# Performance work log

Hardware: AMD Instinct MI355X
Metric: run time of the kernel (lower is better)

The kernel has to match this reference:

```python
import jax, jax.numpy as jnp
import numpy as np

B, C, N = 2, 512, 2048
HEADS, DIM_HEAD, SCALE = 16, 64, 8.0
H_DIM = HEADS * DIM_HEAD
EPS = 1e-12  # F.normalize default eps


def setup_inputs() -> dict:
    key = jax.random.key(0)
    ks = jax.random.split(key, 5)
    x = jax.random.normal(ks[0], (B, C, N), dtype=jnp.float32)
    Wqkv = jax.random.normal(ks[1], (3 * H_DIM, C), dtype=jnp.float32) * (1.0 / np.sqrt(C))
    q_scale = jnp.ones((DIM_HEAD,), dtype=jnp.float32)
    k_scale = jnp.ones((DIM_HEAD,), dtype=jnp.float32)
    Wout = jax.random.normal(ks[2], (C, H_DIM), dtype=jnp.float32) * (1.0 / np.sqrt(H_DIM))
    bout = jax.random.normal(ks[3], (C,), dtype=jnp.float32) * 0.01
    return {"x": x, "Wqkv": Wqkv, "q_scale": q_scale, "k_scale": k_scale,
            "Wout": Wout, "bout": bout}


def _l2norm(t):
    # F.normalize(t, dim=-1): t / max(||t||, eps)
    n = jnp.sqrt(jnp.sum(t * t, axis=-1, keepdims=True))
    return t / jnp.maximum(n, EPS)


def reference(x, Wqkv, q_scale, k_scale, Wout, bout):
    # 1x1 conv == pointwise matmul over channel dim
    qkv = jnp.einsum('oc,bcn->bon', Wqkv, x)              # [B, 3*H_DIM, N]
    q, k, v = jnp.split(qkv, 3, axis=1)
    # unflatten channels -> [B, H, D, N]
    def to_heads(t):
        return t.reshape(B, HEADS, DIM_HEAD, N)
    q, k, v = map(to_heads, (q, k, v))
    # cosine attention: l2-normalize q,k over head dim, apply learned per-dim scales
    q = _l2norm(q.transpose(0, 1, 3, 2)) * q_scale        # [B, H, N, D]
    k = _l2norm(k.transpose(0, 1, 3, 2)) * k_scale        # [B, H, N, D]
    sim = jnp.einsum('bhid,bhjd->bhij', q, k) * SCALE     # [B, H, N, N]
    attn = jax.nn.softmax(sim, axis=-1)
    out = jnp.einsum('bhij,bhdj->bhid', attn, v)          # [B, H, N, D]
    out = out.transpose(0, 1, 3, 2).reshape(B, H_DIM, N)  # b h n d -> b (h d) n
    return jnp.einsum('oc,bcn->bon', Wout, out) + bout[None, :, None]
```

## Files before the change

kernel.cpp:

```cpp
#include <hip/hip_runtime.h>
#include <hip/hip_bf16.h>

#define BATCH 2
#define CCH   512
#define NSEQ  2048
#define HEADS 16
#define DHEAD 64
#define HDIM  1024
#define ODIM  3072
#define QK_PRESCALE 11.541560327111707f

typedef short short4v __attribute__((ext_vector_type(4)));
typedef short short8 __attribute__((ext_vector_type(8)));
typedef float float4v __attribute__((ext_vector_type(4)));

__device__ __forceinline__ unsigned short f2bf(float f) {
    unsigned int u = __float_as_uint(f);
    return (unsigned short)((u + 0x7FFFu + ((u >> 16) & 1u)) >> 16);
}
__device__ __forceinline__ unsigned short f2bf_fast(float f) {
    return (unsigned short)((__float_as_uint(f) + 0x8000u) >> 16);
}
__device__ __forceinline__ float fexp2(float x) {
#if __has_builtin(__builtin_amdgcn_exp2f)
    return __builtin_amdgcn_exp2f(x);
#else
    return exp2f(x);
#endif
}

typedef __attribute__((address_space(1))) const void* as1_cvp;
typedef __attribute__((address_space(3))) void* as3_vp;
__device__ __forceinline__ void cp16(const void* g, void* l) {
    __builtin_amdgcn_global_load_lds((as1_cvp)g, (as3_vp)l, 16, 0, 0);
}

__global__ __launch_bounds__(256) void k_convert_w(
    const float* __restrict__ Wqkv, const float* __restrict__ Wout,
    const float* __restrict__ qs, const float* __restrict__ ks,
    unsigned short* __restrict__ Wqkvb, unsigned short* __restrict__ Woutb,
    float* __restrict__ M) {
    if (blockIdx.x == 0 && threadIdx.x < 64) {
        int lane = threadIdx.x;
        float p = fabsf(qs[lane] * ks[lane]);
#pragma unroll
        for (int off = 1; off < 64; off <<= 1) p = fmaxf(p, __shfl_xor(p, off));
        if (lane == 0) *M = QK_PRESCALE * p;
    }
    int i4 = (blockIdx.x * 256 + threadIdx.x) * 4;
    const float* src; unsigned short* dst; int idx;
    if (i4 < ODIM * CCH) { src = Wqkv; dst = Wqkvb; idx = i4; }
    else { src = Wout; dst = Woutb; idx = i4 - ODIM * CCH; }
    float4 v = *(const float4*)(src + idx);
    ushort4 o;
    o.x = f2bf(v.x); o.y = f2bf(v.y); o.z = f2bf(v.z); o.w = f2bf(v.w);
    *(ushort4*)(dst + idx) = o;
}

__global__ __launch_bounds__(256) void k_transpose_x(
    const float* __restrict__ x, unsigned short* __restrict__ xt) {
    __shared__ unsigned short t[64][65];
    const int b = blockIdx.z, c0 = blockIdx.y * 64, n0 = blockIdx.x * 64;
    const int tr = threadIdx.x >> 6, tc = threadIdx.x & 63;
    const float* xs = x + (size_t)b * CCH * NSEQ;
    unsigned short* xd = xt + (size_t)b * NSEQ * CCH;
#pragma unroll
    for (int r = 0; r < 16; ++r) {
        int c = r * 4 + tr;
        t[c][tc] = f2bf(xs[(size_t)(c0 + c) * NSEQ + n0 + tc]);
    }
    __syncthreads();
#pragma unroll
    for (int r = 0; r < 16; ++r) {
        int n = r * 4 + tr;
        xd[(size_t)(n0 + n) * CCH + c0 + tc] = t[tc][n];
    }
}

__global__ __launch_bounds__(256) void k_gemm_qkv(
    const unsigned short* __restrict__ W, const unsigned short* __restrict__ xt,
    const float* __restrict__ qs, const float* __restrict__ ks,
    unsigned short* __restrict__ qh, unsigned short* __restrict__ kh,
    unsigned short* __restrict__ vb) {
    constexpr int K = CCH, N = NSEQ;
    __shared__ __align__(16) short smem[2 * 128 * 64];
    short* lsA = smem;
    short* lsB = smem + 128 * 64;
    const int tid = threadIdx.x, wave = tid >> 6, lane = tid & 63;
    const int l15 = lane & 15, quad = lane >> 4;
    const int n0 = blockIdx.x * 128, m0 = blockIdx.y * 128, z = blockIdx.z;
    const short* Ab = (const short*)W + (size_t)m0 * K;
    const short* Bb = (const short*)xt + ((size_t)z * N + n0) * K;
    const int wm = wave >> 1, wn = wave & 1;
    const int cswz = (((tid & 7) ^ ((tid >> 3) & 7))) * 8;
    const int sw7 = (l15 & 7);

    float4v acc[4][4];
#pragma unroll
    for (int i = 0; i < 4; ++i)
#pragma unroll
        for (int j = 0; j < 4; ++j) acc[i][j] = (float4v){0.f, 0.f, 0.f, 0.f};

    for (int k0 = 0; k0 < K; k0 += 64) {
#pragma unroll
        for (int it = 0; it < 4; ++it) {
            int row = it * 32 + (tid >> 3);
            cp16(Ab + (size_t)row * K + k0 + cswz, &lsA[it * 2048 + wave * 512]);
            cp16(Bb + (size_t)row * K + k0 + cswz, &lsB[it * 2048 + wave * 512]);
        }
        __syncthreads();
        short8 af[4][2], bfr[4][2];
#pragma unroll
        for (int t = 0; t < 4; ++t)
#pragma unroll
            for (int kk = 0; kk < 2; ++kk) {
                af[t][kk]  = *(const short8*)&lsA[(wm * 64 + t * 16 + l15) * 64 + ((kk * 4 + quad) ^ sw7) * 8];
                bfr[t][kk] = *(const short8*)&lsB[(wn * 64 + t * 16 + l15) * 64 + ((kk * 4 + quad) ^ sw7) * 8];
            }
#pragma unroll
        for (int mt = 0; mt < 4; ++mt)
#pragma unroll
            for (int nt = 0; nt < 4; ++nt) {
                acc[mt][nt] = __builtin_amdgcn_mfma_f32_16x16x32_bf16(af[mt][0], bfr[nt][0], acc[mt][nt], 0, 0, 0);
                acc[mt][nt] = __builtin_amdgcn_mfma_f32_16x16x32_bf16(af[mt][1], bfr[nt][1], acc[mt][nt], 0, 0, 0);
            }
        __syncthreads();
    }

    const int co   = (m0 + wm * 64) >> 6;
    const int part = co >> 4;
    const int h    = co & 15;
    const int bh   = z * HEADS + h;
    short* myT = smem + wave * 4096;

    if (part < 2) {
        float inv[4];
#pragma unroll
        for (int nt = 0; nt < 4; ++nt) {
            float ss = 0.f;
#pragma unroll
            for (int mt = 0; mt < 4; ++mt)
#pragma unroll
                for (int r = 0; r < 4; ++r) ss += acc[mt][nt][r] * acc[mt][nt][r];
            ss += __shfl_xor(ss, 16);
            ss += __shfl_xor(ss, 32);
            inv[nt] = 1.0f / fmaxf(sqrtf(ss), 1e-12f);
        }
        const float* sc = part ? ks : qs;
        const float csc = part ? 1.0f : QK_PRESCALE;
#pragma unroll
        for (int mt = 0; mt < 4; ++mt) {
            const int db = mt * 16 + quad * 4;
            float4 s4 = *(const float4*)(sc + db);
            s4.x *= csc; s4.y *= csc; s4.z *= csc; s4.w *= csc;
#pragma unroll
            for (int nt = 0; nt < 4; ++nt) {
                int nl = nt * 16 + l15;
                short4v o;
                o.x = (short)f2bf(acc[mt][nt][0] * inv[nt] * s4.x);
                o.y = (short)f2bf(acc[mt][nt][1] * inv[nt] * s4.y);
                o.z = (short)f2bf(acc[mt][nt][2] * inv[nt] * s4.z);
                o.w = (short)f2bf(acc[mt][nt][3] * inv[nt] * s4.w);
                *(short4v*)&myT[nl * 64 + (((db >> 3) ^ (nl & 7)) << 3) + (db & 7)] = o;
            }
        }
        unsigned short* dst = (part ? kh : qh) + (size_t)bh * NSEQ * DHEAD
                              + (size_t)(n0 + wn * 64) * DHEAD;
#pragma unroll
        for (int pass = 0; pass < 8; ++pass) {
            int nl = pass * 8 + (lane >> 3), c = lane & 7;
            short8 vv = *(const short8*)&myT[nl * 64 + ((c ^ (nl & 7)) << 3)];
            *(short8*)&dst[(size_t)nl * DHEAD + c * 8] = vv;
        }
    } else {
#pragma unroll
        for (int mt = 0; mt < 4; ++mt)
#pragma unroll
            for (int nt = 0; nt < 4; ++nt) {
                int nl = nt * 16 + l15;
                int swc = nl >> 3, swo = nl & 7;
#pragma unroll
                for (int r = 0; r < 4; ++r) {
                    int d = mt * 16 + quad * 4 + r;
                    myT[d * 64 + ((swc ^ (d & 7)) << 3) + swo] = (short)f2bf(acc[mt][nt][r]);
                }
            }
        unsigned short* dst = vb + (size_t)bh * DHEAD * NSEQ + n0 + wn * 64;
#pragma unroll
        for (int pass = 0; pass < 8; ++pass) {
            int d = pass * 8 + (lane >> 3), c = lane & 7;
            short8 vv = *(const short8*)&myT[d * 64 + ((c ^ (d & 7)) << 3)];
            *(short8*)&dst[(size_t)d * NSEQ + c * 8] = vv;
        }
    }
}

__global__ __launch_bounds__(256, 4) void k_attn(
    const unsigned short* __restrict__ qh, const unsigned short* __restrict__ kh,
    const unsigned short* __restrict__ vb,
    unsigned short* __restrict__ aot, const float* __restrict__ Mptr) {
    __shared__ __align__(16) short Kt[2][64 * 64];
    __shared__ __align__(16) short Vt[2][64 * 64];
    __shared__ __align__(16) short Pt[64 * 64];
    const int tid = threadIdx.x, wave = tid >> 6, lane = tid & 63;
    const int l15 = lane & 15, quad = lane >> 4, q8 = quad * 8;
    const int flat = blockIdx.x;
    const int xcd = flat & 7, idx = flat >> 3;
    const int bh = xcd * 4 + (idx >> 5);
    const int i0 = (idx & 31) * 64;
    const int b = bh >> 4, h = bh & 15;
    const float Ms = *Mptr;
    const float4v mInit = (float4v){-Ms, -Ms, -Ms, -Ms};
    const int cswz = (((tid & 7) ^ ((tid >> 3) & 7))) * 8;
    const int sw7 = (l15 & 7);
    const int srow = tid >> 3;

    short8 qf[2];
    {
        const short* qb = (const short*)qh + ((size_t)bh * NSEQ + i0 + wave * 16) * DHEAD;
        qf[0] = *(const short8*)&qb[l15 * DHEAD + q8];
        qf[1] = *(const short8*)&qb[l15 * DHEAD + 32 + q8];
    }

    float4v of[4];
#pragma unroll
    for (int dt = 0; dt < 4; ++dt) of[dt] = (float4v){0.f, 0.f, 0.f, 0.f};
    float l_acc[4] = {0.f, 0.f, 0.f, 0.f};

    const short* kbase = (const short*)kh + (size_t)bh * NSEQ * DHEAD;
    const short* vbase = (const short*)vb + (size_t)bh * DHEAD * NSEQ;
    short* myP = Pt + wave * 1024;

#pragma unroll
    for (int it = 0; it < 2; ++it) {
        int row = it * 32 + srow;
        cp16(kbase + (size_t)row * DHEAD + cswz, &Kt[0][it * 2048 + wave * 512]);
        cp16(vbase + (size_t)row * NSEQ + cswz, &Vt[0][it * 2048 + wave * 512]);
    }
    __syncthreads();

    int buf = 0;
    for (int j0 = 0; j0 < NSEQ; j0 += 64) {
        if (j0 + 64 < NSEQ) {
            int nb = buf ^ 1;
#pragma unroll
            for (int it = 0; it < 2; ++it) {
                int row = it * 32 + srow;
                cp16(kbase + (size_t)(j0 + 64 + row) * DHEAD + cswz, &Kt[nb][it * 2048 + wave * 512]);
                cp16(vbase + (size_t)row * NSEQ + j0 + 64 + cswz, &Vt[nb][it * 2048 + wave * 512]);
            }
        }

        float4v s[4];
#pragma unroll
        for (int nt = 0; nt < 4; ++nt) {
            short8 kf0 = *(const short8*)&Kt[buf][(nt * 16 + l15) * 64 + ((0 + quad) ^ sw7) * 8];
            short8 kf1 = *(const short8*)&Kt[buf][(nt * 16 + l15) * 64 + ((4 + quad) ^ sw7) * 8];
            float4v zz = mInit;
            zz = __builtin_amdgcn_mfma_f32_16x16x32_bf16(qf[0], kf0, zz, 0, 0, 0);
            zz = __builtin_amdgcn_mfma_f32_16x16x32_bf16(qf[1], kf1, zz, 0, 0, 0);
            s[nt] = zz;
        }

#pragma unroll
        for (int r = 0; r < 4; ++r) {
            int prow = quad * 4 + r;
            int psw = prow & 7;
            float p0 = fexp2(s[0][r]);
            float p1 = fexp2(s[1][r]);
            float p2 = fexp2(s[2][r]);
            float p3 = fexp2(s[3][r]);
            l_acc[r] += (p0 + p1) + (p2 + p3);
            myP[prow * 64 + (((0 + (l15 >> 3)) ^ psw) * 8) + (l15 & 7)] = (short)f2bf_fast(p0);
            myP[prow * 64 + (((2 + (l15 >> 3)) ^ psw) * 8) + (l15 & 7)] = (short)f2bf_fast(p1);
            myP[prow * 64 + (((4 + (l15 >> 3)) ^ psw) * 8) + (l15 & 7)] = (short)f2bf_fast(p2);
            myP[prow * 64 + (((6 + (l15 >> 3)) ^ psw) * 8) + (l15 & 7)] = (short)f2bf_fast(p3);
        }

        short8 af0 = *(const short8*)&myP[l15 * 64 + ((0 + quad) ^ sw7) * 8];
        short8 af1 = *(const short8*)&myP[l15 * 64 + ((4 + quad) ^ sw7) * 8];
#pragma unroll
        for (int dt = 0; dt < 4; ++dt) {
            short8 vf0 = *(const short8*)&Vt[buf][(dt * 16 + l15) * 64 + ((0 + quad) ^ sw7) * 8];
            short8 vf1 = *(const short8*)&Vt[buf][(dt * 16 + l15) * 64 + ((4 + quad) ^ sw7) * 8];
            of[dt] = __builtin_amdgcn_mfma_f32_16x16x32_bf16(af0, vf0, of[dt], 0, 0, 0);
            of[dt] = __builtin_amdgcn_mfma_f32_16x16x32_bf16(af1, vf1, of[dt], 0, 0, 0);
        }

        __syncthreads();
        buf ^= 1;
    }

#pragma unroll
    for (int r = 0; r < 4; ++r) {
        float l = l_acc[r];
        l += __shfl_xor(l, 1); l += __shfl_xor(l, 2);
        l += __shfl_xor(l, 4); l += __shfl_xor(l, 8);
        l_acc[r] = 1.0f / fmaxf(l, 1e-30f);
    }

    unsigned short* ob = aot + ((size_t)b * NSEQ + i0 + wave * 16) * HDIM + h * DHEAD;
#pragma unroll
    for (int dt = 0; dt < 4; ++dt)
#pragma unroll
        for (int r = 0; r < 4; ++r)
            ob[(size_t)(quad * 4 + r) * HDIM + dt * 16 + l15] = f2bf(of[dt][r] * l_acc[r]);
}

__global__ __launch_bounds__(256) void k_gemm_out(
    const unsigned short* __restrict__ W, const unsigned short* __restrict__ aot,
    const float* __restrict__ bias, float* __restrict__ out) {
    constexpr int K = HDIM, N = NSEQ, M = CCH;
    __shared__ __align__(16) short lsA[64 * 64];
    __shared__ __align__(16) short lsB[64 * 64];
    const int tid = threadIdx.x, wave = tid >> 6, lane = tid & 63;
    const int l15 = lane & 15, quad = lane >> 4;
    const int n0 = blockIdx.x * 64, m0 = blockIdx.y * 64, z = blockIdx.z;
    const short* Ab = (const short*)W + (size_t)m0 * K;
    const short* Bb = (const short*)aot + ((size_t)z * N + n0) * K;
    const int wm = wave >> 1, wn = wave & 1;
    const int cswz = (((tid & 7) ^ ((tid >> 3) & 7))) * 8;
    const int sw7 = (l15 & 7);

    float4v acc[2][2];
#pragma unroll
    for (int i = 0; i < 2; ++i)
#pragma unroll
        for (int j = 0; j < 2; ++j) acc[i][j] = (float4v){0.f, 0.f, 0.f, 0.f};

    for (int k0 = 0; k0 < K; k0 += 64) {
        {
            int row = tid >> 3;
            cp16(Ab + (size_t)row * K + k0 + cswz, &lsA[wave * 512]);
            cp16(Ab + (size_t)(row + 32) * K + k0 + cswz, &lsA[2048 + wave * 512]);
            cp16(Bb + (size_t)row * K + k0 + cswz, &lsB[wave * 512]);
            cp16(Bb + (size_t)(row + 32) * K + k0 + cswz, &lsB[2048 + wave * 512]);
        }
        __syncthreads();
        short8 af[2][2], bfr[2][2];
#pragma unroll
        for (int t = 0; t < 2; ++t)
#pragma unroll
            for (int kk = 0; kk < 2; ++kk) {
                af[t][kk]  = *(const short8*)&lsA[(wm * 32 + t * 16 + l15) * 64 + ((kk * 4 + quad) ^ sw7) * 8];
                bfr[t][kk] = *(const short8*)&lsB[(wn * 32 + t * 16 + l15) * 64 + ((kk * 4 + quad) ^ sw7) * 8];
            }
#pragma unroll
        for (int mt = 0; mt < 2; ++mt)
#pragma unroll
            for (int nt = 0; nt < 2; ++nt) {
                acc[mt][nt] = __builtin_amdgcn_mfma_f32_16x16x32_bf16(af[mt][0], bfr[nt][0], acc[mt][nt], 0, 0, 0);
                acc[mt][nt] = __builtin_amdgcn_mfma_f32_16x16x32_bf16(af[mt][1], bfr[nt][1], acc[mt][nt], 0, 0, 0);
            }
        __syncthreads();
    }
    float* Co = out + (size_t)z * M * N;
#pragma unroll
    for (int mt = 0; mt < 2; ++mt)
#pragma unroll
        for (int nt = 0; nt < 2; ++nt) {
            int mrow = m0 + wm * 32 + mt * 16 + quad * 4;
#pragma unroll
            for (int r = 0; r < 4; ++r) {
                int mr = mrow + r;
                int nc = n0 + wn * 32 + nt * 16 + l15;
                Co[(size_t)mr * N + nc] = acc[mt][nt][r] + bias[mr];
            }
        }
}

extern "C" void kernel_launch(void* const* d_in, const int* in_sizes, int n_in,
                              void* d_out, int out_size, void* d_ws, size_t ws_size,
                              hipStream_t stream) {
    const float* x = nullptr; const float* Wqkv = nullptr;
    const float* qs = nullptr; const float* ks = nullptr;
    const float* Wout = nullptr; const float* bout = nullptr;
    for (int i = 0; i < n_in; ++i) {
        switch (in_sizes[i]) {
            case BATCH * CCH * NSEQ: x    = (const float*)d_in[i]; break;
            case ODIM * CCH:         Wqkv = (const float*)d_in[i]; break;
            case CCH * HDIM:         Wout = (const float*)d_in[i]; break;
            case CCH:                bout = (const float*)d_in[i]; break;
            case DHEAD: if (!qs) qs = (const float*)d_in[i]; else ks = (const float*)d_in[i]; break;
            default: break;
        }
    }
    float* y = (float*)d_out;

    char* ws = (char*)d_ws;
    float*          Mbuf  = (float*)(ws + 0);
    unsigned short* Wqkvb = (unsigned short*)(ws + 4096);
    unsigned short* Woutb = (unsigned short*)(ws + 3149824);
    unsigned short* xt    = (unsigned short*)(ws + 4198400);
    unsigned short* qh    = (unsigned short*)(ws + 8392704);
    unsigned short* kh    = (unsigned short*)(ws + 16781312);
    unsigned short* vb    = (unsigned short*)(ws + 25169920);
    unsigned short* aot   = (unsigned short*)(ws + 33558528);

    k_convert_w<<<(ODIM * CCH + CCH * HDIM) / 4 / 256, 256, 0, stream>>>(
        Wqkv, Wout, qs, ks, Wqkvb, Woutb, Mbuf);
    k_transpose_x<<<dim3(NSEQ / 64, CCH / 64, BATCH), 256, 0, stream>>>(x, xt);
    k_gemm_qkv<<<dim3(NSEQ / 128, ODIM / 128, BATCH), 256, 0, stream>>>(Wqkvb, xt, qs, ks, qh, kh, vb);
    k_attn<<<dim3(1024), 256, 0, stream>>>(qh, kh, vb, aot, Mbuf);
    k_gemm_out<<<dim3(NSEQ / 64, CCH / 64, BATCH), 256, 0, stream>>>(Woutb, aot, bout, y);
}
```

Before: 171.0 us.

## Double attention query tile per block and fuse weight-convert with x-transpose

The attention kernel now gives each block 128 query rows, two 16-row m-tiles per wave, so every K/V tile staged in LDS is reused across twice as many queries. This halves the block count and the K/V global and LDS traffic per query. In exchange it uses more registers and LDS per block, and the occupancy hint drops from 4 to 2. Separately, the weight-conversion and x-transpose kernels are merged into one launch to save a kernel launch.

```diff
diff --git a/kernel.cpp b/kernel.cpp
--- a/kernel.cpp
+++ b/kernel.cpp
@@ -35,32 +35,36 @@
     __builtin_amdgcn_global_load_lds((as1_cvp)g, (as3_vp)l, 16, 0, 0);
 }
 
-__global__ __launch_bounds__(256) void k_convert_w(
+__global__ __launch_bounds__(256) void k_prep(
     const float* __restrict__ Wqkv, const float* __restrict__ Wout,
+    const float* __restrict__ x,
     const float* __restrict__ qs, const float* __restrict__ ks,
     unsigned short* __restrict__ Wqkvb, unsigned short* __restrict__ Woutb,
-    float* __restrict__ M) {
-    if (blockIdx.x == 0 && threadIdx.x < 64) {
-        int lane = threadIdx.x;
-        float p = fabsf(qs[lane] * ks[lane]);
-#pragma unroll
-        for (int off = 1; off < 64; off <<= 1) p = fmaxf(p, __shfl_xor(p, off));
-        if (lane == 0) *M = QK_PRESCALE * p;
-    }
-    int i4 = (blockIdx.x * 256 + threadIdx.x) * 4;
-    const float* src; unsigned short* dst; int idx;
-    if (i4 < ODIM * CCH) { src = Wqkv; dst = Wqkvb; idx = i4; }
-    else { src = Wout; dst = Woutb; idx = i4 - ODIM * CCH; }
-    float4 v = *(const float4*)(src + idx);
-    ushort4 o;
-    o.x = f2bf(v.x); o.y = f2bf(v.y); o.z = f2bf(v.z); o.w = f2bf(v.w);
-    *(ushort4*)(dst + idx) = o;
-}
-
-__global__ __launch_bounds__(256) void k_transpose_x(
-    const float* __restrict__ x, unsigned short* __restrict__ xt) {
+    unsigned short* __restrict__ xt, float* __restrict__ M) {
+    const int bx = blockIdx.x;
+    if (bx < 2048) {
+        if (bx == 0 && threadIdx.x < 64) {
+            int lane = threadIdx.x;
+            float p = fabsf(qs[lane] * ks[lane]);
+#pragma unroll
+            for (int off = 1; off < 64; off <<= 1) p = fmaxf(p, __shfl_xor(p, off));
+            if (lane == 0) *M = QK_PRESCALE * p;
+        }
+        int i4 = (bx * 256 + threadIdx.x) * 4;
+        const float* src; unsigned short* dst; int idx;
+        if (i4 < ODIM * CCH) { src = Wqkv; dst = Wqkvb; idx = i4; }
+        else { src = Wout; dst = Woutb; idx = i4 - ODIM * CCH; }
+        float4 v = *(const float4*)(src + idx);
+        ushort4 o;
+        o.x = f2bf(v.x); o.y = f2bf(v.y); o.z = f2bf(v.z); o.w = f2bf(v.w);
+        *(ushort4*)(dst + idx) = o;
+        return;
+    }
     __shared__ unsigned short t[64][65];
-    const int b = blockIdx.z, c0 = blockIdx.y * 64, n0 = blockIdx.x * 64;
+    const int fx = bx - 2048;
+    const int n0 = (fx & 31) * 64;
+    const int c0 = ((fx >> 5) & 7) * 64;
+    const int b  = fx >> 8;
     const int tr = threadIdx.x >> 6, tc = threadIdx.x & 63;
     const float* xs = x + (size_t)b * CCH * NSEQ;
     unsigned short* xd = xt + (size_t)b * NSEQ * CCH;
@@ -195,19 +199,19 @@
     }
 }
 
-__global__ __launch_bounds__(256, 4) void k_attn(
+__global__ __launch_bounds__(256, 2) void k_attn(
     const unsigned short* __restrict__ qh, const unsigned short* __restrict__ kh,
     const unsigned short* __restrict__ vb,
     unsigned short* __restrict__ aot, const float* __restrict__ Mptr) {
     __shared__ __align__(16) short Kt[2][64 * 64];
     __shared__ __align__(16) short Vt[2][64 * 64];
-    __shared__ __align__(16) short Pt[64 * 64];
+    __shared__ __align__(16) short Pt[128 * 64];
     const int tid = threadIdx.x, wave = tid >> 6, lane = tid & 63;
     const int l15 = lane & 15, quad = lane >> 4, q8 = quad * 8;
     const int flat = blockIdx.x;
     const int xcd = flat & 7, idx = flat >> 3;
-    const int bh = xcd * 4 + (idx >> 5);
-    const int i0 = (idx & 31) * 64;
+    const int bh = xcd * 4 + (idx >> 4);
+    const int i0 = (idx & 15) * 128;
     const int b = bh >> 4, h = bh & 15;
     const float Ms = *Mptr;
     const float4v mInit = (float4v){-Ms, -Ms, -Ms, -Ms};
@@ -215,21 +219,29 @@
     const int sw7 = (l15 & 7);
     const int srow = tid >> 3;
 
-    short8 qf[2];
+    short8 qf[2][2];
     {
-        const short* qb = (const short*)qh + ((size_t)bh * NSEQ + i0 + wave * 16) * DHEAD;
-        qf[0] = *(const short8*)&qb[l15 * DHEAD + q8];
-        qf[1] = *(const short8*)&qb[l15 * DHEAD + 32 + q8];
-    }
-
-    float4v of[4];
-#pragma unroll
-    for (int dt = 0; dt < 4; ++dt) of[dt] = (float4v){0.f, 0.f, 0.f, 0.f};
-    float l_acc[4] = {0.f, 0.f, 0.f, 0.f};
+        const short* qb = (const short*)qh + ((size_t)bh * NSEQ + i0 + wave * 32) * DHEAD;
+#pragma unroll
+        for (int mt = 0; mt < 2; ++mt) {
+            qf[mt][0] = *(const short8*)&qb[(mt * 16 + l15) * DHEAD + q8];
+            qf[mt][1] = *(const short8*)&qb[(mt * 16 + l15) * DHEAD + 32 + q8];
+        }
+    }
+
+    float4v of[2][4];
+#pragma unroll
+    for (int mt = 0; mt < 2; ++mt)
+#pragma unroll
+        for (int dt = 0; dt < 4; ++dt) of[mt][dt] = (float4v){0.f, 0.f, 0.f, 0.f};
+    float l_acc[2][4];
+#pragma unroll
+    for (int mt = 0; mt < 2; ++mt)
+#pragma unroll
+        for (int r = 0; r < 4; ++r) l_acc[mt][r] = 0.f;
 
     const short* kbase = (const short*)kh + (size_t)bh * NSEQ * DHEAD;
     const short* vbase = (const short*)vb + (size_t)bh * DHEAD * NSEQ;
-    short* myP = Pt + wave * 1024;
 
 #pragma unroll
     for (int it = 0; it < 2; ++it) {
@@ -251,40 +263,53 @@
             }
         }
 
-        float4v s[4];
+        float4v s[2][4];
 #pragma unroll
         for (int nt = 0; nt < 4; ++nt) {
             short8 kf0 = *(const short8*)&Kt[buf][(nt * 16 + l15) * 64 + ((0 + quad) ^ sw7) * 8];
             short8 kf1 = *(const short8*)&Kt[buf][(nt * 16 + l15) * 64 + ((4 + quad) ^ sw7) * 8];
-            float4v zz = mInit;
-            zz = __builtin_amdgcn_mfma_f32_16x16x32_bf16(qf[0], kf0, zz, 0, 0, 0);
-            zz = __builtin_amdgcn_mfma_f32_16x16x32_bf16(qf[1], kf1, zz, 0, 0, 0);
-            s[nt] = zz;
-        }
-
-#pragma unroll
-        for (int r = 0; r < 4; ++r) {
-            int prow = quad * 4 + r;
-            int psw = prow & 7;
-            float p0 = fexp2(s[0][r]);
-            float p1 = fexp2(s[1][r]);
-            float p2 = fexp2(s[2][r]);
-            float p3 = fexp2(s[3][r]);
-            l_acc[r] += (p0 + p1) + (p2 + p3);
-            myP[prow * 64 + (((0 + (l15 >> 3)) ^ psw) * 8) + (l15 & 7)] = (short)f2bf_fast(p0);
-            myP[prow * 64 + (((2 + (l15 >> 3)) ^ psw) * 8) + (l15 & 7)] = (short)f2bf_fast(p1);
-            myP[prow * 64 + (((4 + (l15 >> 3)) ^ psw) * 8) + (l15 & 7)] = (short)f2bf_fast(p2);
-            myP[prow * 64 + (((6 + (l15 >> 3)) ^ psw) * 8) + (l15 & 7)] = (short)f2bf_fast(p3);
-        }
-
-        short8 af0 = *(const short8*)&myP[l15 * 64 + ((0 + quad) ^ sw7) * 8];
-        short8 af1 = *(const short8*)&myP[l15 * 64 + ((4 + quad) ^ sw7) * 8];
+#pragma unroll
+            for (int mt = 0; mt < 2; ++mt) {
+                float4v zz = mInit;
+                zz = __builtin_amdgcn_mfma_f32_16x16x32_bf16(qf[mt][0], kf0, zz, 0, 0, 0);
+                zz = __builtin_amdgcn_mfma_f32_16x16x32_bf16(qf[mt][1], kf1, zz, 0, 0, 0);
+                s[mt][nt] = zz;
+            }
+        }
+
+#pragma unroll
+        for (int mt = 0; mt < 2; ++mt)
+#pragma unroll
+            for (int r = 0; r < 4; ++r) {
+                int prow = wave * 32 + mt * 16 + quad * 4 + r;
+                int psw = prow & 7;
+                float p0 = fexp2(s[mt][0][r]);
+                float p1 = fexp2(s[mt][1][r]);
+                float p2 = fexp2(s[mt][2][r]);
+                float p3 = fexp2(s[mt][3][r]);
+                l_acc[mt][r] += (p0 + p1) + (p2 + p3);
+                Pt[prow * 64 + (((0 + (l15 >> 3)) ^ psw) * 8) + (l15 & 7)] = (short)f2bf_fast(p0);
+                Pt[prow * 64 + (((2 + (l15 >> 3)) ^ psw) * 8) + (l15 & 7)] = (short)f2bf_fast(p1);
+                Pt[prow * 64 + (((4 + (l15 >> 3)) ^ psw) * 8) + (l15 & 7)] = (short)f2bf_fast(p2);
+                Pt[prow * 64 + (((6 + (l15 >> 3)) ^ psw) * 8) + (l15 & 7)] = (short)f2bf_fast(p3);
+            }
+
+        short8 af0[2], af1[2];
+#pragma unroll
+        for (int mt = 0; mt < 2; ++mt) {
+            int arow = wave * 32 + mt * 16 + l15;
+            af0[mt] = *(const short8*)&Pt[arow * 64 + ((0 + quad) ^ sw7) * 8];
+            af1[mt] = *(const short8*)&Pt[arow * 64 + ((4 + quad) ^ sw7) * 8];
+        }
 #pragma unroll
         for (int dt = 0; dt < 4; ++dt) {
             short8 vf0 = *(const short8*)&Vt[buf][(dt * 16 + l15) * 64 + ((0 + quad) ^ sw7) * 8];
             short8 vf1 = *(const short8*)&Vt[buf][(dt * 16 + l15) * 64 + ((4 + quad) ^ sw7) * 8];
-            of[dt] = __builtin_amdgcn_mfma_f32_16x16x32_bf16(af0, vf0, of[dt], 0, 0, 0);
-            of[dt] = __builtin_amdgcn_mfma_f32_16x16x32_bf16(af1, vf1, of[dt], 0, 0, 0);
+#pragma unroll
+            for (int mt = 0; mt < 2; ++mt) {
+                of[mt][dt] = __builtin_amdgcn_mfma_f32_16x16x32_bf16(af0[mt], vf0, of[mt][dt], 0, 0, 0);
+                of[mt][dt] = __builtin_amdgcn_mfma_f32_16x16x32_bf16(af1[mt], vf1, of[mt][dt], 0, 0, 0);
+            }
         }
 
         __syncthreads();
@@ -292,19 +317,24 @@
     }
 
 #pragma unroll
-    for (int r = 0; r < 4; ++r) {
-        float l = l_acc[r];
-        l += __shfl_xor(l, 1); l += __shfl_xor(l, 2);
-        l += __shfl_xor(l, 4); l += __shfl_xor(l, 8);
-        l_acc[r] = 1.0f / fmaxf(l, 1e-30f);
-    }
-
-    unsigned short* ob = aot + ((size_t)b * NSEQ + i0 + wave * 16) * HDIM + h * DHEAD;
-#pragma unroll
-    for (int dt = 0; dt < 4; ++dt)
-#pragma unroll
-        for (int r = 0; r < 4; ++r)
-            ob[(size_t)(quad * 4 + r) * HDIM + dt * 16 + l15] = f2bf(of[dt][r] * l_acc[r]);
+    for (int mt = 0; mt < 2; ++mt)
+#pragma unroll
+        for (int r = 0; r < 4; ++r) {
+            float l = l_acc[mt][r];
+            l += __shfl_xor(l, 1); l += __shfl_xor(l, 2);
+            l += __shfl_xor(l, 4); l += __shfl_xor(l, 8);
+            l_acc[mt][r] = 1.0f / fmaxf(l, 1e-30f);
+        }
+
+#pragma unroll
+    for (int mt = 0; mt < 2; ++mt) {
+        unsigned short* ob = aot + ((size_t)b * NSEQ + i0 + wave * 32 + mt * 16) * HDIM + h * DHEAD;
+#pragma unroll
+        for (int dt = 0; dt < 4; ++dt)
+#pragma unroll
+            for (int r = 0; r < 4; ++r)
+                ob[(size_t)(quad * 4 + r) * HDIM + dt * 16 + l15] = f2bf(of[mt][dt][r] * l_acc[mt][r]);
+    }
 }
 
 __global__ __launch_bounds__(256) void k_gemm_out(
@@ -397,10 +427,8 @@
     unsigned short* vb    = (unsigned short*)(ws + 25169920);
     unsigned short* aot   = (unsigned short*)(ws + 33558528);
 
-    k_convert_w<<<(ODIM * CCH + CCH * HDIM) / 4 / 256, 256, 0, stream>>>(
-        Wqkv, Wout, qs, ks, Wqkvb, Woutb, Mbuf);
-    k_transpose_x<<<dim3(NSEQ / 64, CCH / 64, BATCH), 256, 0, stream>>>(x, xt);
+    k_prep<<<dim3(2048 + 512), 256, 0, stream>>>(Wqkv, Wout, x, qs, ks, Wqkvb, Woutb, xt, Mbuf);
     k_gemm_qkv<<<dim3(NSEQ / 128, ODIM / 128, BATCH), 256, 0, stream>>>(Wqkvb, xt, qs, ks, qh, kh, vb);
-    k_attn<<<dim3(1024), 256, 0, stream>>>(qh, kh, vb, aot, Mbuf);
+    k_attn<<<dim3(512), 256, 0, stream>>>(qh, kh, vb, aot, Mbuf);
     k_gemm_out<<<dim3(NSEQ / 64, CCH / 64, BATCH), 256, 0, stream>>>(Woutb, aot, bout, y);
 }
```

Result: faster. 161.4 us (-5.6%).
